# Optimization experiments

Hardware: AMD Instinct MI355X
Metric: run time of the kernel (lower is better)

## Reference

```python
import jax, jax.numpy as jnp
import numpy as np

KERNEL = 7
DS_LIM = 0.01
ALPHA_M = 1.0


def _smooth_field(field):
    # field [3,D,H,W] -> depthwise mean filter with kernel 7, SAME padding
    k = KERNEL
    w = jnp.ones((3, 1, k, k, k), dtype=field.dtype) / (k ** 3)
    out = jax.lax.conv_general_dilated(
        field[None], w, (1, 1, 1), 'SAME',
        dimension_numbers=('NCDHW', 'OIDHW', 'NCDHW'),
        feature_group_count=3)
    return out[0]


def _trilinear(vol, coords):
    # vol [B,D,H,W]; coords [B,3,D,H,W] in voxel units
    B, D, H, W = vol.shape
    cz = jnp.clip(coords[:, 0], 0.0, D - 1.0)
    cy = jnp.clip(coords[:, 1], 0.0, H - 1.0)
    cx = jnp.clip(coords[:, 2], 0.0, W - 1.0)
    z0 = jnp.floor(cz).astype(jnp.int32); z1 = jnp.minimum(z0 + 1, D - 1)
    y0 = jnp.floor(cy).astype(jnp.int32); y1 = jnp.minimum(y0 + 1, H - 1)
    x0 = jnp.floor(cx).astype(jnp.int32); x1 = jnp.minimum(x0 + 1, W - 1)
    fz = cz - z0; fy = cy - y0; fx = cx - x0
    b = jnp.arange(B)[:, None, None, None]
    g = lambda zi, yi, xi: vol[b, zi, yi, xi]
    c00 = g(z0, y0, x0) * (1 - fx) + g(z0, y0, x1) * fx
    c01 = g(z0, y1, x0) * (1 - fx) + g(z0, y1, x1) * fx
    c10 = g(z1, y0, x0) * (1 - fx) + g(z1, y0, x1) * fx
    c11 = g(z1, y1, x0) * (1 - fx) + g(z1, y1, x1) * fx
    c0 = c00 * (1 - fy) + c01 * fy
    c1 = c10 * (1 - fy) + c11 * fy
    return c0 * (1 - fz) + c1 * fz


def setup_inputs() -> dict:
    key = jax.random.key(0)
    ks = jax.random.split(key, 8)
    B, C, L = 8, 128, 5
    D = H = W = 96
    return {
        'encode_ds': jax.random.normal(ks[0], (B, C, L, L, L), jnp.float32),
        'orig': jax.random.normal(ks[1], (B, 1, D, H, W), jnp.float32),
        'mask': jax.random.uniform(ks[2], (B, 1, D, H, W), jnp.float32),
        'c1_w': jax.random.normal(ks[3], (1, C, 1, 1, 1), jnp.float32) * 0.05,
        'c1_b': jnp.zeros((1,), jnp.float32),
        'f1_w': jax.random.normal(ks[4], (1, L ** 3), jnp.float32) * 0.1,
        'f1_b': jnp.zeros((1,), jnp.float32),
        'offset_field': jax.random.normal(ks[5], (3, D, H, W), jnp.float32),
    }


def reference(encode_ds, orig, mask, c1_w, c1_b, f1_w, f1_b, offset_field):
    B = encode_ds.shape[0]
    # 1x1x1 Conv3d (128 -> 1) is a per-voxel channel contraction
    a = jnp.einsum('bcdhw,c->bdhw', encode_ds, c1_w[0, :, 0, 0, 0]) + c1_b[0]
    a = a.reshape(B, -1)                                   # [B, 125]
    alpha = jax.nn.sigmoid(a @ f1_w[0] + f1_b[0]) * ALPHA_M  # [B]

    # deform: smoothed, ds_lim-clamped offset field scaled by per-sample alpha
    field = jnp.clip(_smooth_field(offset_field), -DS_LIM, DS_LIM)  # [3,D,H,W]
    _, _, D, H, W = orig.shape
    base = jnp.stack(jnp.meshgrid(jnp.arange(D, dtype=orig.dtype),
                                  jnp.arange(H, dtype=orig.dtype),
                                  jnp.arange(W, dtype=orig.dtype),
                                  indexing='ij'))          # [3,D,H,W]
    scale = jnp.array([D, H, W], orig.dtype).reshape(1, 3, 1, 1, 1)
    disp = alpha[:, None, None, None, None] * field[None] * scale  # [B,3,D,H,W]
    coords = base[None] + disp

    def_ = _trilinear(orig[:, 0], coords)[:, None]
    mask_d = _trilinear(mask[:, 0], coords)[:, None]
    return def_, mask_d
```

## Files before the change

kernel.cpp:

```cpp
#include <hip/hip_runtime.h>
#include <hip/hip_fp16.h>
#include <math.h>

#define DD 96
#define VOX (96*96*96)
#define NB 8
#define NC 128
#define L3 125

#define BTS 16
#define BNT 6
#define BNTILE (BNT*BNT*BNT)
#define BHZ 22
#define BHY 22
#define XSN (BHY * 23 * BTS)

#define TZ 12
#define TY 8
#define TX 32
#define NTZ 8
#define NTY 12
#define NTX 3
#define STILE (NTZ*NTY*NTX)
#define HZS 14
#define HYS 10
#define HXS 34
#define HXP 35
#define HN (HZS*HYS*HXS)
#define HLDS (HZS*HYS*HXP)

typedef float vfloat2 __attribute__((ext_vector_type(2)));
typedef float vfloat4 __attribute__((ext_vector_type(4)));

static __device__ __forceinline__ vfloat2 h2f(__half2 h) {
    float2 t = __half22float2(h);
    vfloat2 r; r.x = t.x; r.y = t.y;
    return r;
}

__global__ __launch_bounds__(256) void blur_alpha(
        const float* __restrict__ in, float* __restrict__ out,
        const float* __restrict__ enc,
        const float* __restrict__ c1_w, const float* __restrict__ c1_b,
        const float* __restrict__ f1_w, const float* __restrict__ f1_b,
        float* __restrict__ alpha) {
    __shared__ float xs[XSN];
    __shared__ float red[4];
    int tid = threadIdx.x;

    if (blockIdx.x >= 3 * BNTILE) {
        int b = blockIdx.x - 3 * BNTILE;
        const float4* e4 = (const float4*)(enc + (size_t)b * NC * L3);
        float s = 0.f;
        for (int j = tid; j < (NC * L3) / 4; j += 256) {
            float4 v = e4[j];
            int f = j * 4;
            s += v.x * c1_w[(f + 0) / L3] * f1_w[(f + 0) % L3];
            s += v.y * c1_w[(f + 1) / L3] * f1_w[(f + 1) % L3];
            s += v.z * c1_w[(f + 2) / L3] * f1_w[(f + 2) % L3];
            s += v.w * c1_w[(f + 3) / L3] * f1_w[(f + 3) % L3];
        }
        for (int off = 32; off > 0; off >>= 1) s += __shfl_down(s, off, 64);
        int lane = tid & 63, wid = tid >> 6;
        if (lane == 0) red[wid] = s;
        __syncthreads();
        if (tid == 0) {
            float tot = red[0] + red[1] + red[2] + red[3];
            float fwsum = 0.f;
            for (int v = 0; v < L3; ++v) fwsum += f1_w[v];
            float x = tot + c1_b[0] * fwsum + f1_b[0];
            alpha[b] = 1.f / (1.f + expf(-x));
        }
        return;
    }

    int blk = blockIdx.x;
    int c = blk / BNTILE;
    int t = blk % BNTILE;
    int tz = t / (BNT * BNT), ty = (t / BNT) % BNT, tx = t % BNT;
    int bz = tz * BTS, by = ty * BTS, bx = tx * BTS;
    const float* ib = in + (size_t)c * VOX;

    bool xedge = (bx == 0) || (bx == DD - BTS);
    for (int i = tid; i < BHY * BHZ * BTS; i += 256) {
        int hy = i / (BHZ * BTS);
        int r2 = i - hy * (BHZ * BTS);
        int hz = r2 >> 4;
        int xo = r2 & 15;
        int gz = bz + hz - 3, gy = by + hy - 3;
        float s = 0.f;
        if ((unsigned)gz < DD && (unsigned)gy < DD) {
            const float* p = ib + (gz * DD + gy) * DD + (bx + xo - 3);
            if (!xedge) {
                #pragma unroll
                for (int dx = 0; dx < 7; ++dx) s += p[dx];
            } else {
                int gx0 = bx + xo - 3;
                #pragma unroll
                for (int dx = 0; dx < 7; ++dx)
                    if ((unsigned)(gx0 + dx) < DD) s += p[dx];
            }
        }
        xs[(hy * 23 + hz) * 16 + xo] = s;
    }
    __syncthreads();

    for (int cc = tid; cc < BHZ * BTS; cc += 256) {
        int hz = cc >> 4, xo = cc & 15;
        int base = hz * 16 + xo;
        float s = 0.f;
        #pragma unroll
        for (int hy = 0; hy < 7; ++hy) s += xs[hy * 368 + base];
        #pragma unroll
        for (int yo = 0; yo < 16; ++yo) {
            float old = xs[yo * 368 + base];
            float nxt = (yo < 15) ? xs[(yo + 7) * 368 + base] : 0.f;
            xs[yo * 368 + base] = s;
            s += nxt - old;
        }
    }
    __syncthreads();

    {
        int yo = tid >> 4, xo = tid & 15;
        int base = yo * 368 + xo;
        float s = 0.f;
        #pragma unroll
        for (int hz = 0; hz < 7; ++hz) s += xs[base + hz * 16];
        float* ob = out + (size_t)c * VOX + (by + yo) * DD + bx + xo;
        #pragma unroll
        for (int zo = 0; zo < 16; ++zo) {
            float v = s * (1.0f / 343.0f);
            v = fminf(fmaxf(v, -0.01f), 0.01f) * 96.0f;
            ob[(size_t)(bz + zo) * DD * DD] = v;
            s += xs[base + (zo + 7) * 16] - xs[base + zo * 16];
        }
    }
}

__global__ __launch_bounds__(256, 8) void sample_tile(
        const float* __restrict__ orig,
        const float* __restrict__ mask,
        const float* __restrict__ field,
        const float* __restrict__ alpha,
        float* __restrict__ out) {
    __shared__ __half2 tile[HLDS];

    int blk = blockIdx.x;
    int b = blk / STILE;
    int r = blk % STILE;
    int o = r & 7;
    int l = r >> 3;
    int zh = o >> 2;
    int yq = o & 3;
    int lz4 = l / 9, ly3 = (l / 3) % 3, lx3 = l % 3;
    int tz = zh * 4 + lz4;
    int ty = yq * 3 + ly3;
    int tx = lx3;
    int bz = tz * TZ, by = ty * TY, bx = tx * TX;

    const float* ob = orig + (size_t)b * VOX;
    const float* mb = mask + (size_t)b * VOX;
    int tid = threadIdx.x;

    for (int i = tid; i < HN; i += 256) {
        int hz = i / (HYS * HXS);
        int rr = i - hz * (HYS * HXS);
        int hy = rr / HXS;
        int hx = rr - hy * HXS;
        int gz = min(max(bz + hz - 1, 0), DD - 1);
        int gy = min(max(by + hy - 1, 0), DD - 1);
        int gx = min(max(bx + hx - 1, 0), DD - 1);
        int g = (gz * DD + gy) * DD + gx;
        tile[(hz * HYS + hy) * HXP + hx] = __floats2half2_rn(ob[g], mb[g]);
    }
    float a = alpha[b];
    __syncthreads();

    const vfloat4* fz4 = (const vfloat4*)field;
    const vfloat4* fy4 = (const vfloat4*)(field + VOX);
    const vfloat4* fx4 = (const vfloat4*)(field + 2 * VOX);
    vfloat4* oD = (vfloat4*)(out);
    vfloat4* oM = (vfloat4*)(out + (size_t)NB * VOX);

    int lz  = tid >> 6;
    int ly  = (tid >> 3) & 7;
    int lxq = tid & 7;
    int gy  = by + ly;
    int gx0 = bx + 4 * lxq;
    float gyf = (float)gy;
    float gx0f = (float)gx0;
    float c1z = (float)(1 - bz), c1y = (float)(1 - by), c1x = (float)(1 - bx);

    auto samp = [&](float gzf, float dzv, float dyv, float dxv,
                    float gxf) -> vfloat2 {
        float cz = fminf(fmaxf(fmaf(a, dzv, gzf), 0.f), (float)(DD - 1)) + c1z;
        float cy = fminf(fmaxf(fmaf(a, dyv, gyf), 0.f), (float)(DD - 1)) + c1y;
        float cx = fminf(fmaxf(fmaf(a, dxv, gxf), 0.f), (float)(DD - 1)) + c1x;
        float flz = floorf(cz), fly = floorf(cy), flx = floorf(cx);
        float fzf = cz - flz, fyf = cy - fly, fxf = cx - flx;
        int iz = (int)flz, iy = (int)fly, ix = (int)flx;

        const __half2* tp = tile + (iz * HYS + iy) * HXP + ix;
        vfloat2 v000 = h2f(tp[0]);
        vfloat2 v001 = h2f(tp[1]);
        vfloat2 v010 = h2f(tp[HXP]);
        vfloat2 v011 = h2f(tp[HXP + 1]);
        vfloat2 v100 = h2f(tp[HYS * HXP]);
        vfloat2 v101 = h2f(tp[HYS * HXP + 1]);
        vfloat2 v110 = h2f(tp[(HYS + 1) * HXP]);
        vfloat2 v111 = h2f(tp[(HYS + 1) * HXP + 1]);

        vfloat2 FX = {fxf, fxf}, FY = {fyf, fyf}, FZ = {fzf, fzf};
        vfloat2 c00 = v000 + FX * (v001 - v000);
        vfloat2 c01 = v010 + FX * (v011 - v010);
        vfloat2 c10 = v100 + FX * (v101 - v100);
        vfloat2 c11 = v110 + FX * (v111 - v110);
        vfloat2 c0 = c00 + FY * (c01 - c00);
        vfloat2 c1 = c10 + FY * (c11 - c10);
        return c0 + FZ * (c1 - c0);
    };

    int vp4 = (((bz + lz) * DD + gy) * DD + gx0) >> 2;
    vfloat4 dz = fz4[vp4], dy = fy4[vp4], dx = fx4[vp4];
    size_t ob0 = (size_t)b * (VOX / 4);

    #pragma unroll
    for (int it = 0; it < TZ / 4; ++it) {
        vfloat4 dzn = {0,0,0,0}, dyn = {0,0,0,0}, dxn = {0,0,0,0};
        if (it < TZ / 4 - 1) {
            int vq = vp4 + DD * DD;
            dzn = fz4[vq]; dyn = fy4[vq]; dxn = fx4[vq];
        }
        float gzf = (float)(bz + 4 * it + lz);

        vfloat2 r0 = samp(gzf, dz.x, dy.x, dx.x, gx0f);
        vfloat2 r1 = samp(gzf, dz.y, dy.y, dx.y, gx0f + 1.f);
        vfloat2 r2 = samp(gzf, dz.z, dy.z, dx.z, gx0f + 2.f);
        vfloat2 r3 = samp(gzf, dz.w, dy.w, dx.w, gx0f + 3.f);

        vfloat4 vD = {r0.x, r1.x, r2.x, r3.x};
        vfloat4 vM = {r0.y, r1.y, r2.y, r3.y};
        __builtin_nontemporal_store(vD, &oD[ob0 + vp4]);
        __builtin_nontemporal_store(vM, &oM[ob0 + vp4]);

        vp4 += DD * DD;
        dz = dzn; dy = dyn; dx = dxn;
    }
}

extern "C" void kernel_launch(void* const* d_in, const int* in_sizes, int n_in,
                              void* d_out, int out_size, void* d_ws, size_t ws_size,
                              hipStream_t stream) {
    const float* enc   = (const float*)d_in[0];
    const float* orig  = (const float*)d_in[1];
    const float* mask  = (const float*)d_in[2];
    const float* c1_w  = (const float*)d_in[3];
    const float* c1_b  = (const float*)d_in[4];
    const float* f1_w  = (const float*)d_in[5];
    const float* f1_b  = (const float*)d_in[6];
    const float* offs  = (const float*)d_in[7];
    float* out = (float*)d_out;

    float* ws = (float*)d_ws;
    float* alpha = ws;
    float* fieldB = ws + 16;

    blur_alpha<<<3 * BNTILE + NB, 256, 0, stream>>>(
        offs, fieldB, enc, c1_w, c1_b, f1_w, f1_b, alpha);
    sample_tile<<<NB * STILE, 256, 0, stream>>>(orig, mask, fieldB, alpha, out);
}
```

Before: 182.4 us.

## Sample directly from global memory instead of a shared-memory half2 halo tile

Removes the per-block staging of a padded half-precision orig/mask halo tile into LDS along with its barrier. Trilinear samples now read pairs of adjacent fp32 values straight from global memory with 8-byte loads and rely on the caches for reuse. Indices are clamped to DD-2 so each pair load stays in bounds. This drops the LDS fill cost and the fp16 rounding, but each sample now issues eight global or cache loads, which may raise memory latency pressure.

Result: slower. 202.8 us (+11.2%).

```diff
diff --git a/kernel.cpp b/kernel.cpp
--- a/kernel.cpp
+++ b/kernel.cpp
@@ -22,21 +22,10 @@
 #define NTY 12
 #define NTX 3
 #define STILE (NTZ*NTY*NTX)
-#define HZS 14
-#define HYS 10
-#define HXS 34
-#define HXP 35
-#define HN (HZS*HYS*HXS)
-#define HLDS (HZS*HYS*HXP)
 
 typedef float vfloat2 __attribute__((ext_vector_type(2)));
 typedef float vfloat4 __attribute__((ext_vector_type(4)));
-
-static __device__ __forceinline__ vfloat2 h2f(__half2 h) {
-    float2 t = __half22float2(h);
-    vfloat2 r; r.x = t.x; r.y = t.y;
-    return r;
-}
+typedef float f2u __attribute__((ext_vector_type(2), aligned(4)));
 
 __global__ __launch_bounds__(256) void blur_alpha(
         const float* __restrict__ in, float* __restrict__ out,
@@ -144,8 +133,6 @@
         const float* __restrict__ field,
         const float* __restrict__ alpha,
         float* __restrict__ out) {
-    __shared__ __half2 tile[HLDS];
-
     int blk = blockIdx.x;
     int b = blk / STILE;
     int r = blk % STILE;
@@ -162,20 +149,7 @@
     const float* ob = orig + (size_t)b * VOX;
     const float* mb = mask + (size_t)b * VOX;
     int tid = threadIdx.x;
-
-    for (int i = tid; i < HN; i += 256) {
-        int hz = i / (HYS * HXS);
-        int rr = i - hz * (HYS * HXS);
-        int hy = rr / HXS;
-        int hx = rr - hy * HXS;
-        int gz = min(max(bz + hz - 1, 0), DD - 1);
-        int gy = min(max(by + hy - 1, 0), DD - 1);
-        int gx = min(max(bx + hx - 1, 0), DD - 1);
-        int g = (gz * DD + gy) * DD + gx;
-        tile[(hz * HYS + hy) * HXP + hx] = __floats2half2_rn(ob[g], mb[g]);
-    }
     float a = alpha[b];
-    __syncthreads();
 
     const vfloat4* fz4 = (const vfloat4*)field;
     const vfloat4* fy4 = (const vfloat4*)(field + VOX);
@@ -190,35 +164,46 @@
     int gx0 = bx + 4 * lxq;
     float gyf = (float)gy;
     float gx0f = (float)gx0;
-    float c1z = (float)(1 - bz), c1y = (float)(1 - by), c1x = (float)(1 - bx);
 
     auto samp = [&](float gzf, float dzv, float dyv, float dxv,
                     float gxf) -> vfloat2 {
-        float cz = fminf(fmaxf(fmaf(a, dzv, gzf), 0.f), (float)(DD - 1)) + c1z;
-        float cy = fminf(fmaxf(fmaf(a, dyv, gyf), 0.f), (float)(DD - 1)) + c1y;
-        float cx = fminf(fmaxf(fmaf(a, dxv, gxf), 0.f), (float)(DD - 1)) + c1x;
-        float flz = floorf(cz), fly = floorf(cy), flx = floorf(cx);
-        float fzf = cz - flz, fyf = cy - fly, fxf = cx - flx;
-        int iz = (int)flz, iy = (int)fly, ix = (int)flx;
-
-        const __half2* tp = tile + (iz * HYS + iy) * HXP + ix;
-        vfloat2 v000 = h2f(tp[0]);
-        vfloat2 v001 = h2f(tp[1]);
-        vfloat2 v010 = h2f(tp[HXP]);
-        vfloat2 v011 = h2f(tp[HXP + 1]);
-        vfloat2 v100 = h2f(tp[HYS * HXP]);
-        vfloat2 v101 = h2f(tp[HYS * HXP + 1]);
-        vfloat2 v110 = h2f(tp[(HYS + 1) * HXP]);
-        vfloat2 v111 = h2f(tp[(HYS + 1) * HXP + 1]);
-
-        vfloat2 FX = {fxf, fxf}, FY = {fyf, fyf}, FZ = {fzf, fzf};
-        vfloat2 c00 = v000 + FX * (v001 - v000);
-        vfloat2 c01 = v010 + FX * (v011 - v010);
-        vfloat2 c10 = v100 + FX * (v101 - v100);
-        vfloat2 c11 = v110 + FX * (v111 - v110);
-        vfloat2 c0 = c00 + FY * (c01 - c00);
-        vfloat2 c1 = c10 + FY * (c11 - c10);
-        return c0 + FZ * (c1 - c0);
+        float cz = fminf(fmaxf(fmaf(a, dzv, gzf), 0.f), 95.f);
+        float cy = fminf(fmaxf(fmaf(a, dyv, gyf), 0.f), 95.f);
+        float cx = fminf(fmaxf(fmaf(a, dxv, gxf), 0.f), 95.f);
+        int iz = min((int)cz, DD - 2);
+        int iy = min((int)cy, DD - 2);
+        int ix = min((int)cx, DD - 2);
+        float fzf = cz - (float)iz;
+        float fyf = cy - (float)iy;
+        float fxf = cx - (float)ix;
+        int t = iz * (DD * DD) + iy * DD + ix;
+
+        f2u o00 = *(const f2u*)(ob + t);
+        f2u o01 = *(const f2u*)(ob + t + DD);
+        f2u o10 = *(const f2u*)(ob + t + DD * DD);
+        f2u o11 = *(const f2u*)(ob + t + DD * DD + DD);
+        f2u m00 = *(const f2u*)(mb + t);
+        f2u m01 = *(const f2u*)(mb + t + DD);
+        f2u m10 = *(const f2u*)(mb + t + DD * DD);
+        f2u m11 = *(const f2u*)(mb + t + DD * DD + DD);
+
+        float qx = 1.f - fxf, qy = 1.f - fyf, qz = 1.f - fzf;
+        float c00 = o00.x * qx + o00.y * fxf;
+        float c01 = o01.x * qx + o01.y * fxf;
+        float c10 = o10.x * qx + o10.y * fxf;
+        float c11 = o11.x * qx + o11.y * fxf;
+        float d00 = m00.x * qx + m00.y * fxf;
+        float d01 = m01.x * qx + m01.y * fxf;
+        float d10 = m10.x * qx + m10.y * fxf;
+        float d11 = m11.x * qx + m11.y * fxf;
+        float c0 = c00 * qy + c01 * fyf;
+        float c1 = c10 * qy + c11 * fyf;
+        float d0 = d00 * qy + d01 * fyf;
+        float d1 = d10 * qy + d11 * fyf;
+        vfloat2 rv;
+        rv.x = c0 * qz + c1 * fzf;
+        rv.y = d0 * qz + d1 * fzf;
+        return rv;
     };
 
     int vp4 = (((bz + lz) * DD + gy) * DD + gx0) >> 2;
```
